# Kernel optimization log

Hardware: AMD Instinct MI355X
Metric: run time of the kernel (lower is better)

Reference implementation:

```python
import jax, jax.numpy as jnp
import numpy as np

ALPHA = 1.0
EPS = 1e-8

def setup_inputs() -> dict:
    key = jax.random.key(0)
    k1, k2, k3 = jax.random.split(key, 3)
    B, L, S, H, E, D = 4, 2048, 2048, 8, 64, 64
    queries = jax.random.normal(k1, (B, L, H, E), dtype=jnp.float32)
    keys = jax.random.normal(k2, (B, S, H, E), dtype=jnp.float32)
    values = jax.random.normal(k3, (B, S, H, D), dtype=jnp.float32)
    return {"queries": queries, "keys": keys, "values": values}

def reference(queries, keys, values):
    E = queries.shape[3]
    scale = 1.0 / jnp.sqrt(jnp.asarray(E, queries.dtype))
    # dot_product: [B,H,L,S]
    dot = jnp.einsum('blhe,bshe->bhls', queries, keys)
    q_norm2 = jnp.sum(queries ** 2, axis=-1).transpose(0, 2, 1)[..., :, None]  # [B,H,L,1]
    k_norm2 = jnp.sum(keys ** 2, axis=-1).transpose(0, 2, 1)[..., None, :]     # [B,H,1,S]
    wedge2 = jax.nn.relu(q_norm2 * k_norm2 - dot ** 2)
    wedge = jnp.sqrt(wedge2 + EPS)
    scores = ((1.0 - ALPHA) * dot + ALPHA * wedge) * scale
    A = jax.nn.softmax(scores, axis=-1)  # dropout in eval mode = identity
    out = jnp.einsum('bhls,bshd->blhd', A, values)
    return out
```

## Files before the change

### kernel.cpp

```cpp
#include <hip/hip_runtime.h>

typedef __attribute__((ext_vector_type(2))) float f32x2;
typedef __attribute__((ext_vector_type(4))) float f32x4;
typedef __attribute__((ext_vector_type(4))) float float4v;
typedef __attribute__((ext_vector_type(8))) short bf16x8;
typedef __attribute__((ext_vector_type(8))) unsigned short ushort8;

#define DEVI static __device__ __forceinline__

namespace {
constexpr int kL = 2048, kS = 2048, kH = 8;
constexpr int QB = 64, KVB = 64, NKT = kS / KVB;
constexpr float kC = 0.18033688f;
constexpr int KTILE = 8448;
constexpr int VTILE = 8192;
constexpr int KBH = 32 * KTILE;
constexpr int VBH = 32 * VTILE;
}

DEVI int swz(int byteoff) { return byteoff ^ (((byteoff >> 7) & 7) << 4); }

DEVI unsigned cvtpk(float lo, float hi) {
  unsigned r;
  asm("v_cvt_pk_bf16_f32 %0, %1, %2" : "=v"(r) : "v"(lo), "v"(hi));
  return r;
}

__global__ __launch_bounds__(256) void prep_k(const float* __restrict__ Kg,
                                              char* __restrict__ Kb) {
  const int chunk = (int)blockIdx.x * 256 + (int)threadIdx.x;
  const int tile = chunk >> 9;
  const int i = chunk & 511;
  const int bh = tile >> 5, kt = tile & 31;
  const int b = bh >> 3, h = bh & 7;
  const int row = i >> 3;
  const int colsel = (i & 7) ^ (row & 7);
  const int s = kt * 64 + row;
  const float* src = Kg + (((size_t)b * kS + s) * kH + h) * 64 + colsel * 8;
  float4v v0 = *(const float4v*)(src);
  float4v v1 = *(const float4v*)(src + 4);
  float pn = v0.x*v0.x + v0.y*v0.y + v0.z*v0.z + v0.w*v0.w
           + v1.x*v1.x + v1.y*v1.y + v1.z*v1.z + v1.w*v1.w;
  union { unsigned w[4]; ushort8 u; } o;
  o.w[0] = cvtpk(v0.x, v0.y); o.w[1] = cvtpk(v0.z, v0.w);
  o.w[2] = cvtpk(v1.x, v1.y); o.w[3] = cvtpk(v1.z, v1.w);
  char* tb = Kb + (size_t)tile * KTILE;
  *(ushort8*)(tb + i * 16) = o.u;
  pn += __shfl_xor(pn, 1);
  pn += __shfl_xor(pn, 2);
  pn += __shfl_xor(pn, 4);
  if ((i & 7) == 0) *(float*)(tb + 8192 + row * 4) = pn;
}

__global__ __launch_bounds__(256) void prep_v(const float* __restrict__ Vg,
                                              char* __restrict__ Vt) {
  __shared__ char tile[64 * 128];
  const int t = (int)threadIdx.x;
  const int bid = (int)blockIdx.x;
  const int st = bid & 31, bh = bid >> 5;
  const int b = bh >> 3, h = bh & 7;
  {
    const int sl = t >> 2, c0 = (t & 3) * 16;
    const float* src = Vg + (((size_t)b * kS + st * 64 + sl) * kH + h) * 64 + c0;
    float4v v0 = *(const float4v*)(src);
    float4v v1 = *(const float4v*)(src + 4);
    float4v v2 = *(const float4v*)(src + 8);
    float4v v3 = *(const float4v*)(src + 12);
    union { unsigned w[4]; ushort8 u; } t0, t1;
    t0.w[0] = cvtpk(v0.x, v0.y); t0.w[1] = cvtpk(v0.z, v0.w);
    t0.w[2] = cvtpk(v1.x, v1.y); t0.w[3] = cvtpk(v1.z, v1.w);
    t1.w[0] = cvtpk(v2.x, v2.y); t1.w[1] = cvtpk(v2.z, v2.w);
    t1.w[2] = cvtpk(v3.x, v3.y); t1.w[3] = cvtpk(v3.z, v3.w);
    *(ushort8*)(tile + swz(sl * 128 + c0 * 2)) = t0.u;
    *(ushort8*)(tile + swz(sl * 128 + c0 * 2 + 16)) = t1.u;
  }
  __syncthreads();
  char* dst = Vt + (size_t)bid * VTILE;
#pragma unroll
  for (int cc = 0; cc < 2; ++cc) {
    const int i = t * 2 + cc;
    const int z = swz(i * 16);
    const int d = z >> 7;
    const int k0 = ((z >> 4) & 7) * 8;
    union { unsigned short s[8]; ushort8 u; } o;
#pragma unroll
    for (int j = 0; j < 8; ++j) {
      const int k = k0 + j;
      const int sig = (((k >> 5) * 2 + ((k & 7) >> 2)) << 4) |
                      (((k >> 3) & 3) << 2) | (k & 3);
      o.s[j] = *(const unsigned short*)(tile + swz(sig * 128 + d * 2));
    }
    *(ushort8*)(dst + i * 16) = o.u;
  }
}

__global__ __launch_bounds__(256, 4) void geo_attn_kernel(
    const float* __restrict__ Qg, const char* __restrict__ Kb,
    const char* __restrict__ Vt, float* __restrict__ Og) {
  __shared__ char lds[2][16384];

  const int t = (int)threadIdx.x;
  const int wv = t >> 6, lane = t & 63, gg = lane >> 4, cl = lane & 15;
  const int n = (int)blockIdx.x;
  const int bh = (n & 7) * 4 + ((n >> 3) & 3);
  const int l0 = (n >> 5) * QB;
  const int b = bh >> 3, h = bh & 7;

  const int q = l0 + wv * 16 + cl;
  const float* qp = Qg + (((size_t)b * kL + q) * kH + h) * 64;
  float4v x0 = *(const float4v*)(qp + gg * 8);
  float4v x1 = *(const float4v*)(qp + gg * 8 + 4);
  float4v x2 = *(const float4v*)(qp + gg * 8 + 32);
  float4v x3 = *(const float4v*)(qp + gg * 8 + 36);
  x0 *= kC; x1 *= kC; x2 *= kC; x3 *= kC;
  float pn = 0.f;
#pragma unroll
  for (int j = 0; j < 4; ++j) {
    pn = fmaf(x0[j], x0[j], pn); pn = fmaf(x1[j], x1[j], pn);
    pn = fmaf(x2[j], x2[j], pn); pn = fmaf(x3[j], x3[j], pn);
  }
  union frag { bf16x8 v; unsigned w[4]; };
  frag qb0, qb1;
  qb0.w[0] = cvtpk(x0.x, x0.y); qb0.w[1] = cvtpk(x0.z, x0.w);
  qb0.w[2] = cvtpk(x1.x, x1.y); qb0.w[3] = cvtpk(x1.z, x1.w);
  qb1.w[0] = cvtpk(x2.x, x2.y); qb1.w[1] = cvtpk(x2.z, x2.w);
  qb1.w[2] = cvtpk(x3.x, x3.y); qb1.w[3] = cvtpk(x3.z, x3.w);
  pn += __shfl_xor(pn, 16);
  pn += __shfl_xor(pn, 32);
  const f32x2 qn2p = {pn, pn};

  frag vone;
  vone.w[0] = vone.w[1] = vone.w[2] = vone.w[3] = 0x3F803F80u;

  const bool isK = (wv < 2);
  const char* gp = (isK ? Kb + (size_t)bh * KBH : Vt + (size_t)bh * VBH)
                   + (wv & 1) * 4096 + lane * 16;
  const int gstride = isK ? KTILE : VTILE;
  const char* ktail = Kb + (size_t)bh * KBH + 8192;

#define STAGE(BUF) do { \
    char* _lb = lds[BUF] + wv * 4096; \
    __builtin_amdgcn_global_load_lds((__attribute__((address_space(1))) void*)(gp),        (__attribute__((address_space(3))) void*)(_lb),        16, 0, 0); \
    __builtin_amdgcn_global_load_lds((__attribute__((address_space(1))) void*)(gp + 1024), (__attribute__((address_space(3))) void*)(_lb + 1024), 16, 0, 0); \
    __builtin_amdgcn_global_load_lds((__attribute__((address_space(1))) void*)(gp + 2048), (__attribute__((address_space(3))) void*)(_lb + 2048), 16, 0, 0); \
    __builtin_amdgcn_global_load_lds((__attribute__((address_space(1))) void*)(gp + 3072), (__attribute__((address_space(3))) void*)(_lb + 3072), 16, 0, 0); \
  } while (0)

  f32x4 oacc[4];
#pragma unroll
  for (int dt = 0; dt < 4; ++dt) oacc[dt] = (f32x4){0.f, 0.f, 0.f, 0.f};
  f32x4 lacc = (f32x4){0.f, 0.f, 0.f, 0.f};

  STAGE(0);
  gp += gstride;
  float4v kn2r[4];
#pragma unroll
  for (int nt = 0; nt < 4; ++nt)
    kn2r[nt] = *(const float4v*)(ktail + nt * 64 + gg * 16);
  ktail += KTILE;
  __syncthreads();

  int cur = 0;
  for (int kt = 0; kt < NKT; ++kt) {
    if (kt + 1 < NKT) { STAGE(cur ^ 1); gp += gstride; }

    float4v kn2n[4];
#pragma unroll
    for (int nt = 0; nt < 4; ++nt)
      kn2n[nt] = *(const float4v*)(ktail + nt * 64 + gg * 16);
    ktail += KTILE;

    const char* ksc = lds[cur];
    const char* vsc = lds[cur] + 8192;

    f32x4 dacc[4];
#pragma unroll
    for (int nt = 0; nt < 4; ++nt) {
      bf16x8 ka0 = *(const bf16x8*)(ksc + swz((nt * 16 + cl) * 128 + gg * 16));
      bf16x8 ka1 = *(const bf16x8*)(ksc + swz((nt * 16 + cl) * 128 + gg * 16 + 64));
      f32x4 acc = {0.f, 0.f, 0.f, 0.f};
      acc = __builtin_amdgcn_mfma_f32_16x16x32_bf16(ka0, qb0.v, acc, 0, 0, 0);
      acc = __builtin_amdgcn_mfma_f32_16x16x32_bf16(ka1, qb1.v, acc, 0, 0, 0);
      dacc[nt] = acc;
    }

    unsigned pw[8];
#pragma unroll
    for (int i = 0; i < 8; ++i) {
      const int nt = i >> 1, hh = (i & 1) * 2;
      const f32x2 d2 = {dacc[nt][hh], dacc[nt][hh + 1]};
      const f32x2 k2 = {kn2r[nt][hh], kn2r[nt][hh + 1]};
      const f32x2 w2 = qn2p * k2 - d2 * d2;
      const float p0 = __builtin_amdgcn_exp2f(__builtin_amdgcn_sqrtf(fabsf(w2.x)));
      const float p1 = __builtin_amdgcn_exp2f(__builtin_amdgcn_sqrtf(fabsf(w2.y)));
      pw[i] = cvtpk(p0, p1);
    }
    frag pa0, pa1;
    pa0.w[0] = pw[0]; pa0.w[1] = pw[1]; pa0.w[2] = pw[2]; pa0.w[3] = pw[3];
    pa1.w[0] = pw[4]; pa1.w[1] = pw[5]; pa1.w[2] = pw[6]; pa1.w[3] = pw[7];

#pragma unroll
    for (int dt = 0; dt < 4; ++dt) {
      bf16x8 vb0 = *(const bf16x8*)(vsc + swz((dt * 16 + cl) * 128 + gg * 16));
      bf16x8 vb1 = *(const bf16x8*)(vsc + swz((dt * 16 + cl) * 128 + gg * 16 + 64));
      f32x4 acc = oacc[dt];
      acc = __builtin_amdgcn_mfma_f32_16x16x32_bf16(pa0.v, vb0, acc, 0, 0, 0);
      acc = __builtin_amdgcn_mfma_f32_16x16x32_bf16(pa1.v, vb1, acc, 0, 0, 0);
      oacc[dt] = acc;
    }
    lacc = __builtin_amdgcn_mfma_f32_16x16x32_bf16(pa0.v, vone.v, lacc, 0, 0, 0);
    lacc = __builtin_amdgcn_mfma_f32_16x16x32_bf16(pa1.v, vone.v, lacc, 0, 0, 0);

#pragma unroll
    for (int nt = 0; nt < 4; ++nt) kn2r[nt] = kn2n[nt];

    __syncthreads();
    cur ^= 1;
  }
#undef STAGE

#pragma unroll
  for (int r = 0; r < 4; ++r) {
    const int l = l0 + wv * 16 + gg * 4 + r;
    const float inv = 1.f / lacc[r];
    float* op = Og + (((size_t)b * kL + l) * kH + h) * 64;
#pragma unroll
    for (int dt = 0; dt < 4; ++dt)
      op[dt * 16 + cl] = oacc[dt][r] * inv;
  }
}

extern "C" void kernel_launch(void* const* d_in, const int* in_sizes, int n_in,
                              void* d_out, int out_size, void* d_ws, size_t ws_size,
                              hipStream_t stream) {
  const float* Qg = (const float*)d_in[0];
  const float* Kg = (const float*)d_in[1];
  const float* Vg = (const float*)d_in[2];
  float* Og = (float*)d_out;
  char* Kb = (char*)d_ws;
  char* Vt = (char*)d_ws + (size_t)1024 * KTILE;
  prep_k<<<2048, 256, 0, stream>>>(Kg, Kb);
  prep_v<<<1024, 256, 0, stream>>>(Vg, Vt);
  geo_attn_kernel<<<dim3(1024), dim3(256), 0, stream>>>(Qg, Kb, Vt, Og);
}
```

Baseline: 74.66 us.

## Stage K norms through LDS and interleave softmax with PV MFMAs using setprio

```diff
diff --git a/kernel.cpp b/kernel.cpp
--- a/kernel.cpp
+++ b/kernel.cpp
@@ -1,6 +1,5 @@
 #include <hip/hip_runtime.h>
 
-typedef __attribute__((ext_vector_type(2))) float f32x2;
 typedef __attribute__((ext_vector_type(4))) float f32x4;
 typedef __attribute__((ext_vector_type(4))) float float4v;
 typedef __attribute__((ext_vector_type(8))) short bf16x8;
@@ -16,6 +15,7 @@
 constexpr int VTILE = 8192;
 constexpr int KBH = 32 * KTILE;
 constexpr int VBH = 32 * VTILE;
+constexpr int LBUF = KTILE + VTILE;
 }
 
 DEVI int swz(int byteoff) { return byteoff ^ (((byteoff >> 7) & 7) << 4); }
@@ -97,7 +97,7 @@
 __global__ __launch_bounds__(256, 4) void geo_attn_kernel(
     const float* __restrict__ Qg, const char* __restrict__ Kb,
     const char* __restrict__ Vt, float* __restrict__ Og) {
-  __shared__ char lds[2][16384];
+  __shared__ char lds[2][LBUF];
 
   const int t = (int)threadIdx.x;
   const int wv = t >> 6, lane = t & 63, gg = lane >> 4, cl = lane & 15;
@@ -127,7 +127,7 @@
   qb1.w[2] = cvtpk(x3.x, x3.y); qb1.w[3] = cvtpk(x3.z, x3.w);
   pn += __shfl_xor(pn, 16);
   pn += __shfl_xor(pn, 32);
-  const f32x2 qn2p = {pn, pn};
+  const float qn2 = pn;
 
   frag vone;
   vone.w[0] = vone.w[1] = vone.w[2] = vone.w[3] = 0x3F803F80u;
@@ -136,14 +136,17 @@
   const char* gp = (isK ? Kb + (size_t)bh * KBH : Vt + (size_t)bh * VBH)
                    + (wv & 1) * 4096 + lane * 16;
   const int gstride = isK ? KTILE : VTILE;
-  const char* ktail = Kb + (size_t)bh * KBH + 8192;
+  const char* gt = Kb + (size_t)bh * KBH + 8192 + lane * 4;
+  const int ldsoff = isK ? (wv & 1) * 4096 : KTILE + (wv & 1) * 4096;
 
 #define STAGE(BUF) do { \
-    char* _lb = lds[BUF] + wv * 4096; \
+    char* _lb = lds[BUF] + ldsoff; \
     __builtin_amdgcn_global_load_lds((__attribute__((address_space(1))) void*)(gp),        (__attribute__((address_space(3))) void*)(_lb),        16, 0, 0); \
     __builtin_amdgcn_global_load_lds((__attribute__((address_space(1))) void*)(gp + 1024), (__attribute__((address_space(3))) void*)(_lb + 1024), 16, 0, 0); \
     __builtin_amdgcn_global_load_lds((__attribute__((address_space(1))) void*)(gp + 2048), (__attribute__((address_space(3))) void*)(_lb + 2048), 16, 0, 0); \
     __builtin_amdgcn_global_load_lds((__attribute__((address_space(1))) void*)(gp + 3072), (__attribute__((address_space(3))) void*)(_lb + 3072), 16, 0, 0); \
+    if (wv == 0) \
+      __builtin_amdgcn_global_load_lds((__attribute__((address_space(1))) void*)(gt), (__attribute__((address_space(3))) void*)(lds[BUF] + 8192 + lane * 4), 4, 0, 0); \
   } while (0)
 
   f32x4 oacc[4];
@@ -152,28 +155,23 @@
   f32x4 lacc = (f32x4){0.f, 0.f, 0.f, 0.f};
 
   STAGE(0);
-  gp += gstride;
-  float4v kn2r[4];
-#pragma unroll
-  for (int nt = 0; nt < 4; ++nt)
-    kn2r[nt] = *(const float4v*)(ktail + nt * 64 + gg * 16);
-  ktail += KTILE;
+  gp += gstride; gt += KTILE;
   __syncthreads();
 
   int cur = 0;
   for (int kt = 0; kt < NKT; ++kt) {
-    if (kt + 1 < NKT) { STAGE(cur ^ 1); gp += gstride; }
-
-    float4v kn2n[4];
+    if (kt + 1 < NKT) { STAGE(cur ^ 1); gp += gstride; gt += KTILE; }
+
+    const char* ksc = lds[cur];
+    const char* vsc = lds[cur] + KTILE;
+
+    float4v kn2v[4];
 #pragma unroll
     for (int nt = 0; nt < 4; ++nt)
-      kn2n[nt] = *(const float4v*)(ktail + nt * 64 + gg * 16);
-    ktail += KTILE;
-
-    const char* ksc = lds[cur];
-    const char* vsc = lds[cur] + 8192;
+      kn2v[nt] = *(const float4v*)(ksc + 8192 + nt * 64 + gg * 16);
 
     f32x4 dacc[4];
+    __builtin_amdgcn_s_setprio(1);
 #pragma unroll
     for (int nt = 0; nt < 4; ++nt) {
       bf16x8 ka0 = *(const bf16x8*)(ksc + swz((nt * 16 + cl) * 128 + gg * 16));
@@ -183,36 +181,53 @@
       acc = __builtin_amdgcn_mfma_f32_16x16x32_bf16(ka1, qb1.v, acc, 0, 0, 0);
       dacc[nt] = acc;
     }
-
-    unsigned pw[8];
-#pragma unroll
-    for (int i = 0; i < 8; ++i) {
-      const int nt = i >> 1, hh = (i & 1) * 2;
-      const f32x2 d2 = {dacc[nt][hh], dacc[nt][hh + 1]};
-      const f32x2 k2 = {kn2r[nt][hh], kn2r[nt][hh + 1]};
-      const f32x2 w2 = qn2p * k2 - d2 * d2;
-      const float p0 = __builtin_amdgcn_exp2f(__builtin_amdgcn_sqrtf(fabsf(w2.x)));
-      const float p1 = __builtin_amdgcn_exp2f(__builtin_amdgcn_sqrtf(fabsf(w2.y)));
-      pw[i] = cvtpk(p0, p1);
+    __builtin_amdgcn_s_setprio(0);
+
+    bf16x8 vb0[4], vb1[4];
+#pragma unroll
+    for (int dt = 0; dt < 4; ++dt) {
+      vb0[dt] = *(const bf16x8*)(vsc + swz((dt * 16 + cl) * 128 + gg * 16));
+      vb1[dt] = *(const bf16x8*)(vsc + swz((dt * 16 + cl) * 128 + gg * 16 + 64));
     }
-    frag pa0, pa1;
-    pa0.w[0] = pw[0]; pa0.w[1] = pw[1]; pa0.w[2] = pw[2]; pa0.w[3] = pw[3];
-    pa1.w[0] = pw[4]; pa1.w[1] = pw[5]; pa1.w[2] = pw[6]; pa1.w[3] = pw[7];
-
-#pragma unroll
-    for (int dt = 0; dt < 4; ++dt) {
-      bf16x8 vb0 = *(const bf16x8*)(vsc + swz((dt * 16 + cl) * 128 + gg * 16));
-      bf16x8 vb1 = *(const bf16x8*)(vsc + swz((dt * 16 + cl) * 128 + gg * 16 + 64));
-      f32x4 acc = oacc[dt];
-      acc = __builtin_amdgcn_mfma_f32_16x16x32_bf16(pa0.v, vb0, acc, 0, 0, 0);
-      acc = __builtin_amdgcn_mfma_f32_16x16x32_bf16(pa1.v, vb1, acc, 0, 0, 0);
-      oacc[dt] = acc;
-    }
+
+    float sc[4][4];
+#pragma unroll
+    for (int nt = 0; nt < 2; ++nt)
+#pragma unroll
+      for (int r = 0; r < 4; ++r) {
+        const float d = dacc[nt][r];
+        const float w2 = fmaf(-d, d, qn2 * kn2v[nt][r]);
+        sc[nt][r] = __builtin_amdgcn_exp2f(__builtin_amdgcn_sqrtf(fabsf(w2)));
+      }
+    frag pa0;
+    pa0.w[0] = cvtpk(sc[0][0], sc[0][1]); pa0.w[1] = cvtpk(sc[0][2], sc[0][3]);
+    pa0.w[2] = cvtpk(sc[1][0], sc[1][1]); pa0.w[3] = cvtpk(sc[1][2], sc[1][3]);
+
+    __builtin_amdgcn_s_setprio(1);
+#pragma unroll
+    for (int dt = 0; dt < 4; ++dt)
+      oacc[dt] = __builtin_amdgcn_mfma_f32_16x16x32_bf16(pa0.v, vb0[dt], oacc[dt], 0, 0, 0);
     lacc = __builtin_amdgcn_mfma_f32_16x16x32_bf16(pa0.v, vone.v, lacc, 0, 0, 0);
+    __builtin_amdgcn_s_setprio(0);
+
+#pragma unroll
+    for (int nt = 2; nt < 4; ++nt)
+#pragma unroll
+      for (int r = 0; r < 4; ++r) {
+        const float d = dacc[nt][r];
+        const float w2 = fmaf(-d, d, qn2 * kn2v[nt][r]);
+        sc[nt][r] = __builtin_amdgcn_exp2f(__builtin_amdgcn_sqrtf(fabsf(w2)));
+      }
+    frag pa1;
+    pa1.w[0] = cvtpk(sc[2][0], sc[2][1]); pa1.w[1] = cvtpk(sc[2][2], sc[2][3]);
+    pa1.w[2] = cvtpk(sc[3][0], sc[3][1]); pa1.w[3] = cvtpk(sc[3][2], sc[3][3]);
+
+    __builtin_amdgcn_s_setprio(1);
+#pragma unroll
+    for (int dt = 0; dt < 4; ++dt)
+      oacc[dt] = __builtin_amdgcn_mfma_f32_16x16x32_bf16(pa1.v, vb1[dt], oacc[dt], 0, 0, 0);
     lacc = __builtin_amdgcn_mfma_f32_16x16x32_bf16(pa1.v, vone.v, lacc, 0, 0, 0);
-
-#pragma unroll
-    for (int nt = 0; nt < 4; ++nt) kn2r[nt] = kn2n[nt];
+    __builtin_amdgcn_s_setprio(0);
 
     __syncthreads();
     cur ^= 1;
```

Measured after the change: 71.00 us. 4.9% less time.

## Stage key norms via LDS, unroll double-buffer loop, split softmax-PV into halves with setprio

Applied to the files above, without the earlier changes.

```diff
diff --git a/kernel.cpp b/kernel.cpp
--- a/kernel.cpp
+++ b/kernel.cpp
@@ -1,6 +1,5 @@
 #include <hip/hip_runtime.h>
 
-typedef __attribute__((ext_vector_type(2))) float f32x2;
 typedef __attribute__((ext_vector_type(4))) float f32x4;
 typedef __attribute__((ext_vector_type(4))) float float4v;
 typedef __attribute__((ext_vector_type(8))) short bf16x8;
@@ -16,6 +15,7 @@
 constexpr int VTILE = 8192;
 constexpr int KBH = 32 * KTILE;
 constexpr int VBH = 32 * VTILE;
+constexpr int LBUF = KTILE + VTILE;
 }
 
 DEVI int swz(int byteoff) { return byteoff ^ (((byteoff >> 7) & 7) << 4); }
@@ -97,7 +97,7 @@
 __global__ __launch_bounds__(256, 4) void geo_attn_kernel(
     const float* __restrict__ Qg, const char* __restrict__ Kb,
     const char* __restrict__ Vt, float* __restrict__ Og) {
-  __shared__ char lds[2][16384];
+  __shared__ char lds[2 * LBUF];
 
   const int t = (int)threadIdx.x;
   const int wv = t >> 6, lane = t & 63, gg = lane >> 4, cl = lane & 15;
@@ -127,23 +127,34 @@
   qb1.w[2] = cvtpk(x3.x, x3.y); qb1.w[3] = cvtpk(x3.z, x3.w);
   pn += __shfl_xor(pn, 16);
   pn += __shfl_xor(pn, 32);
-  const f32x2 qn2p = {pn, pn};
+  const float qn2 = pn;
 
   frag vone;
   vone.w[0] = vone.w[1] = vone.w[2] = vone.w[3] = 0x3F803F80u;
+
+  const char* pA = lds + ((cl * 128 + gg * 16) ^ ((cl & 7) << 4));
+  const char* pB = lds + ((cl * 128 + gg * 16 + 64) ^ ((cl & 7) << 4));
+  const char* pT = lds + gg * 16;
 
   const bool isK = (wv < 2);
   const char* gp = (isK ? Kb + (size_t)bh * KBH : Vt + (size_t)bh * VBH)
                    + (wv & 1) * 4096 + lane * 16;
   const int gstride = isK ? KTILE : VTILE;
-  const char* ktail = Kb + (size_t)bh * KBH + 8192;
-
-#define STAGE(BUF) do { \
-    char* _lb = lds[BUF] + wv * 4096; \
-    __builtin_amdgcn_global_load_lds((__attribute__((address_space(1))) void*)(gp),        (__attribute__((address_space(3))) void*)(_lb),        16, 0, 0); \
-    __builtin_amdgcn_global_load_lds((__attribute__((address_space(1))) void*)(gp + 1024), (__attribute__((address_space(3))) void*)(_lb + 1024), 16, 0, 0); \
-    __builtin_amdgcn_global_load_lds((__attribute__((address_space(1))) void*)(gp + 2048), (__attribute__((address_space(3))) void*)(_lb + 2048), 16, 0, 0); \
-    __builtin_amdgcn_global_load_lds((__attribute__((address_space(1))) void*)(gp + 3072), (__attribute__((address_space(3))) void*)(_lb + 3072), 16, 0, 0); \
+  const char* gt = Kb + (size_t)bh * KBH + 8192 + lane * 4;
+  const int ldsoff = isK ? (wv & 1) * 4096 : KTILE + (wv & 1) * 4096;
+  char* const sd0 = lds + ldsoff;
+  char* const sd1 = lds + LBUF + ldsoff;
+  char* const st0 = lds + 8192 + lane * 4;
+  char* const st1 = lds + LBUF + 8192 + lane * 4;
+
+#define STAGE(SD, ST) do { \
+    __builtin_amdgcn_global_load_lds((__attribute__((address_space(1))) void*)(gp),        (__attribute__((address_space(3))) void*)(SD),        16, 0, 0); \
+    __builtin_amdgcn_global_load_lds((__attribute__((address_space(1))) void*)(gp + 1024), (__attribute__((address_space(3))) void*)((SD) + 1024), 16, 0, 0); \
+    __builtin_amdgcn_global_load_lds((__attribute__((address_space(1))) void*)(gp + 2048), (__attribute__((address_space(3))) void*)((SD) + 2048), 16, 0, 0); \
+    __builtin_amdgcn_global_load_lds((__attribute__((address_space(1))) void*)(gp + 3072), (__attribute__((address_space(3))) void*)((SD) + 3072), 16, 0, 0); \
+    if (wv == 0) \
+      __builtin_amdgcn_global_load_lds((__attribute__((address_space(1))) void*)(gt), (__attribute__((address_space(3))) void*)(ST), 4, 0, 0); \
+    gp += gstride; gt += KTILE; \
   } while (0)
 
   f32x4 oacc[4];
@@ -151,73 +162,67 @@
   for (int dt = 0; dt < 4; ++dt) oacc[dt] = (f32x4){0.f, 0.f, 0.f, 0.f};
   f32x4 lacc = (f32x4){0.f, 0.f, 0.f, 0.f};
 
-  STAGE(0);
-  gp += gstride;
-  float4v kn2r[4];
-#pragma unroll
-  for (int nt = 0; nt < 4; ++nt)
-    kn2r[nt] = *(const float4v*)(ktail + nt * 64 + gg * 16);
-  ktail += KTILE;
+#define BODY(BO) do { \
+    float4v kn2v[4]; \
+    _Pragma("unroll") for (int nt = 0; nt < 4; ++nt) \
+      kn2v[nt] = *(const float4v*)(pT + (BO) + 8192 + nt * 64); \
+    f32x4 dacc[4]; \
+    __builtin_amdgcn_s_setprio(1); \
+    _Pragma("unroll") for (int nt = 0; nt < 4; ++nt) { \
+      bf16x8 ka0 = *(const bf16x8*)(pA + (BO) + nt * 2048); \
+      bf16x8 ka1 = *(const bf16x8*)(pB + (BO) + nt * 2048); \
+      f32x4 acc = {0.f, 0.f, 0.f, 0.f}; \
+      acc = __builtin_amdgcn_mfma_f32_16x16x32_bf16(ka0, qb0.v, acc, 0, 0, 0); \
+      acc = __builtin_amdgcn_mfma_f32_16x16x32_bf16(ka1, qb1.v, acc, 0, 0, 0); \
+      dacc[nt] = acc; } \
+    __builtin_amdgcn_s_setprio(0); \
+    bf16x8 vb0[4], vb1[4]; \
+    _Pragma("unroll") for (int dt = 0; dt < 4; ++dt) { \
+      vb0[dt] = *(const bf16x8*)(pA + (BO) + KTILE + dt * 2048); \
+      vb1[dt] = *(const bf16x8*)(pB + (BO) + KTILE + dt * 2048); } \
+    float sc[4][4]; \
+    _Pragma("unroll") for (int nt = 0; nt < 2; ++nt) \
+      _Pragma("unroll") for (int r = 0; r < 4; ++r) { \
+        const float d = dacc[nt][r]; \
+        const float w2 = fmaf(-d, d, qn2 * kn2v[nt][r]); \
+        sc[nt][r] = __builtin_amdgcn_exp2f(__builtin_amdgcn_sqrtf(fabsf(w2))); } \
+    frag pa0; \
+    pa0.w[0] = cvtpk(sc[0][0], sc[0][1]); pa0.w[1] = cvtpk(sc[0][2], sc[0][3]); \
+    pa0.w[2] = cvtpk(sc[1][0], sc[1][1]); pa0.w[3] = cvtpk(sc[1][2], sc[1][3]); \
+    __builtin_amdgcn_s_setprio(1); \
+    _Pragma("unroll") for (int dt = 0; dt < 4; ++dt) \
+      oacc[dt] = __builtin_amdgcn_mfma_f32_16x16x32_bf16(pa0.v, vb0[dt], oacc[dt], 0, 0, 0); \
+    lacc = __builtin_amdgcn_mfma_f32_16x16x32_bf16(pa0.v, vone.v, lacc, 0, 0, 0); \
+    __builtin_amdgcn_s_setprio(0); \
+    _Pragma("unroll") for (int nt = 2; nt < 4; ++nt) \
+      _Pragma("unroll") for (int r = 0; r < 4; ++r) { \
+        const float d = dacc[nt][r]; \
+        const float w2 = fmaf(-d, d, qn2 * kn2v[nt][r]); \
+        sc[nt][r] = __builtin_amdgcn_exp2f(__builtin_amdgcn_sqrtf(fabsf(w2))); } \
+    frag pa1; \
+    pa1.w[0] = cvtpk(sc[2][0], sc[2][1]); pa1.w[1] = cvtpk(sc[2][2], sc[2][3]); \
+    pa1.w[2] = cvtpk(sc[3][0], sc[3][1]); pa1.w[3] = cvtpk(sc[3][2], sc[3][3]); \
+    __builtin_amdgcn_s_setprio(1); \
+    _Pragma("unroll") for (int dt = 0; dt < 4; ++dt) \
+      oacc[dt] = __builtin_amdgcn_mfma_f32_16x16x32_bf16(pa1.v, vb1[dt], oacc[dt], 0, 0, 0); \
+    lacc = __builtin_amdgcn_mfma_f32_16x16x32_bf16(pa1.v, vone.v, lacc, 0, 0, 0); \
+    __builtin_amdgcn_s_setprio(0); \
+  } while (0)
+
+  STAGE(sd0, st0);
   __syncthreads();
 
-  int cur = 0;
-  for (int kt = 0; kt < NKT; ++kt) {
-    if (kt + 1 < NKT) { STAGE(cur ^ 1); gp += gstride; }
-
-    float4v kn2n[4];
-#pragma unroll
-    for (int nt = 0; nt < 4; ++nt)
-      kn2n[nt] = *(const float4v*)(ktail + nt * 64 + gg * 16);
-    ktail += KTILE;
-
-    const char* ksc = lds[cur];
-    const char* vsc = lds[cur] + 8192;
-
-    f32x4 dacc[4];
-#pragma unroll
-    for (int nt = 0; nt < 4; ++nt) {
-      bf16x8 ka0 = *(const bf16x8*)(ksc + swz((nt * 16 + cl) * 128 + gg * 16));
-      bf16x8 ka1 = *(const bf16x8*)(ksc + swz((nt * 16 + cl) * 128 + gg * 16 + 64));
-      f32x4 acc = {0.f, 0.f, 0.f, 0.f};
-      acc = __builtin_amdgcn_mfma_f32_16x16x32_bf16(ka0, qb0.v, acc, 0, 0, 0);
-      acc = __builtin_amdgcn_mfma_f32_16x16x32_bf16(ka1, qb1.v, acc, 0, 0, 0);
-      dacc[nt] = acc;
-    }
-
-    unsigned pw[8];
-#pragma unroll
-    for (int i = 0; i < 8; ++i) {
-      const int nt = i >> 1, hh = (i & 1) * 2;
-      const f32x2 d2 = {dacc[nt][hh], dacc[nt][hh + 1]};
-      const f32x2 k2 = {kn2r[nt][hh], kn2r[nt][hh + 1]};
-      const f32x2 w2 = qn2p * k2 - d2 * d2;
-      const float p0 = __builtin_amdgcn_exp2f(__builtin_amdgcn_sqrtf(fabsf(w2.x)));
-      const float p1 = __builtin_amdgcn_exp2f(__builtin_amdgcn_sqrtf(fabsf(w2.y)));
-      pw[i] = cvtpk(p0, p1);
-    }
-    frag pa0, pa1;
-    pa0.w[0] = pw[0]; pa0.w[1] = pw[1]; pa0.w[2] = pw[2]; pa0.w[3] = pw[3];
-    pa1.w[0] = pw[4]; pa1.w[1] = pw[5]; pa1.w[2] = pw[6]; pa1.w[3] = pw[7];
-
-#pragma unroll
-    for (int dt = 0; dt < 4; ++dt) {
-      bf16x8 vb0 = *(const bf16x8*)(vsc + swz((dt * 16 + cl) * 128 + gg * 16));
-      bf16x8 vb1 = *(const bf16x8*)(vsc + swz((dt * 16 + cl) * 128 + gg * 16 + 64));
-      f32x4 acc = oacc[dt];
-      acc = __builtin_amdgcn_mfma_f32_16x16x32_bf16(pa0.v, vb0, acc, 0, 0, 0);
-      acc = __builtin_amdgcn_mfma_f32_16x16x32_bf16(pa1.v, vb1, acc, 0, 0, 0);
-      oacc[dt] = acc;
-    }
-    lacc = __builtin_amdgcn_mfma_f32_16x16x32_bf16(pa0.v, vone.v, lacc, 0, 0, 0);
-    lacc = __builtin_amdgcn_mfma_f32_16x16x32_bf16(pa1.v, vone.v, lacc, 0, 0, 0);
-
-#pragma unroll
-    for (int nt = 0; nt < 4; ++nt) kn2r[nt] = kn2n[nt];
-
+#pragma unroll 1
+  for (int it = 0; it < NKT / 2; ++it) {
+    STAGE(sd1, st1);
+    BODY(0);
     __syncthreads();
-    cur ^= 1;
+    if (it + 1 < NKT / 2) STAGE(sd0, st0);
+    BODY(LBUF);
+    __syncthreads();
   }
 #undef STAGE
+#undef BODY
 
 #pragma unroll
   for (int r = 0; r < 4; ++r) {
```

Measured after the change: 69.17 us. 7.4% less time.
